# Optimization experiments

Hardware: AMD Instinct MI355X
Metric: run time of the kernel (lower is better)

Reference implementation:

```python
import jax, jax.numpy as jnp
import numpy as np

D_EMBED = 1024
D_CROSS = 768
N_HEADS = 16
D_HEAD = D_EMBED // N_HEADS


def setup_inputs() -> dict:
    key = jax.random.key(0)
    ks = jax.random.split(key, 10)
    s = 0.02
    return {
        "x": jax.random.normal(ks[0], (4, 4096, D_EMBED), dtype=jnp.float32),
        "y": jax.random.normal(ks[1], (4, 1024, D_CROSS), dtype=jnp.float32),
        "Wq": jax.random.normal(ks[2], (D_EMBED, D_EMBED), dtype=jnp.float32) * s,
        "bq": jnp.zeros((D_EMBED,), dtype=jnp.float32),
        "Wk": jax.random.normal(ks[3], (D_CROSS, D_EMBED), dtype=jnp.float32) * s,
        "bk": jnp.zeros((D_EMBED,), dtype=jnp.float32),
        "Wv": jax.random.normal(ks[4], (D_CROSS, D_EMBED), dtype=jnp.float32) * s,
        "bv": jnp.zeros((D_EMBED,), dtype=jnp.float32),
        "Wo": jax.random.normal(ks[5], (D_EMBED, D_EMBED), dtype=jnp.float32) * s,
        "bo": jnp.zeros((D_EMBED,), dtype=jnp.float32),
    }


def reference(x, y, Wq, bq, Wk, bk, Wv, bv, Wo, bo):
    b, sq, _ = x.shape
    skv = y.shape[1]
    # projections
    q = x @ Wq + bq   # [b, sq, d_embed]
    k = y @ Wk + bk   # [b, skv, d_embed]
    v = y @ Wv + bv   # [b, skv, d_embed]
    # split heads: [b, h, s, d_head]
    q = q.reshape(b, sq, N_HEADS, D_HEAD).transpose(0, 2, 1, 3)
    k = k.reshape(b, skv, N_HEADS, D_HEAD).transpose(0, 2, 1, 3)
    v = v.reshape(b, skv, N_HEADS, D_HEAD).transpose(0, 2, 1, 3)
    scale = 1.0 / jnp.sqrt(jnp.float32(D_HEAD))
    scores = jnp.einsum("bhqd,bhkd->bhqk", q, k) * scale
    attn = jax.nn.softmax(scores, axis=-1)
    out = jnp.einsum("bhqk,bhkd->bhqd", attn, v)
    out = out.transpose(0, 2, 1, 3).reshape(b, sq, D_EMBED)
    return out @ Wo + bo
```

## Files before the change

kernel.cpp:

```cpp
#include <hip/hip_runtime.h>

typedef unsigned short ushort_t;
typedef __attribute__((ext_vector_type(8))) __bf16 bf16x8;
typedef __attribute__((ext_vector_type(4))) float floatx4;
typedef __attribute__((ext_vector_type(8))) unsigned short ushortx8;
typedef __attribute__((ext_vector_type(4))) unsigned short ushortx4;
typedef __attribute__((ext_vector_type(4))) short short4v;
typedef __attribute__((ext_vector_type(2))) unsigned uint2v;

__device__ __forceinline__ ushort_t f2bf(float f) {
    union { float f; unsigned u; } v; v.f = f;
    unsigned r = v.u + 0x7fffu + ((v.u >> 16) & 1u);
    return (ushort_t)(r >> 16);
}

__device__ __forceinline__ void gld_lds16(const ushort_t* g, ushort_t* l) {
    __builtin_amdgcn_global_load_lds(
        (const __attribute__((address_space(1))) unsigned*)g,
        (__attribute__((address_space(3))) unsigned*)l, 16, 0, 0);
}

__device__ __forceinline__ unsigned pk_bf16(float a, float b) {
    unsigned ua = __builtin_bit_cast(unsigned, a) + 0x8000u;
    unsigned ub = __builtin_bit_cast(unsigned, b) + 0x8000u;
    return __builtin_amdgcn_perm(ub, ua, 0x07060302u);
}

__global__ __launch_bounds__(256) void prep(
    const float* __restrict__ x, const float* __restrict__ y,
    const float* __restrict__ Wq, const float* __restrict__ Wo,
    const float* __restrict__ Wk, const float* __restrict__ Wv,
    ushort_t* __restrict__ xb, ushort_t* __restrict__ yb,
    ushort_t* __restrict__ Wqt, ushort_t* __restrict__ Wot,
    ushort_t* __restrict__ Wkvt) {
    const int bid = blockIdx.x;
    if (bid < 19456) {
        const int NX = 4194304;
        int i = bid * 256 + threadIdx.x;
        float4 v; ushortx4* dst;
        if (i < NX) { v = ((const float4*)x)[i]; dst = (ushortx4*)xb + i; }
        else        { int j = i - NX; v = ((const float4*)y)[j]; dst = (ushortx4*)yb + j; }
        ushortx4 o;
        o.x = f2bf(v.x); o.y = f2bf(v.y); o.z = f2bf(v.z); o.w = f2bf(v.w);
        *dst = o;
        return;
    }
    __shared__ ushort_t t[32][33];
    const float* W; ushort_t* Wt; int K, n0, k0;
    if (bid < 21504) {
        int tt = bid - 19456;
        W = (tt >> 10) ? Wo : Wq;
        Wt = (tt >> 10) ? Wot : Wqt;
        K = 1024;
        int r = tt & 1023;
        n0 = (r & 31) * 32; k0 = (r >> 5) * 32;
    } else {
        int tt = bid - 21504;
        int z = tt / 768, r = tt - z * 768;
        W = z ? Wv : Wk;
        Wt = Wkvt + (size_t)z * 786432;
        K = 768;
        n0 = (r & 31) * 32; k0 = (r >> 5) * 32;
    }
    const int tx = threadIdx.x & 31, ty = threadIdx.x >> 5;
#pragma unroll
    for (int i = 0; i < 4; ++i)
        t[ty + 8 * i][tx] = f2bf(W[(size_t)(k0 + ty + 8 * i) * 1024 + n0 + tx]);
    __syncthreads();
#pragma unroll
    for (int i = 0; i < 4; ++i)
        Wt[(size_t)(n0 + ty + 8 * i) * K + k0 + tx] = t[tx][ty + 8 * i];
}

__device__ __forceinline__ void gemm_core(
    const ushort_t* __restrict__ A, const ushort_t* __restrict__ Bt,
    int K, int m0, int n0, ushort_t* As, ushort_t* Bs,
    floatx4 (&acc)[4][4], int tid, int wr, int wc, int quad, int l16) {
    const ushort_t* ga0 = A + (size_t)(m0 + (tid >> 2)) * K + (tid & 3) * 8;
    const ushort_t* ga1 = A + (size_t)(m0 + 64 + (tid >> 2)) * K + (tid & 3) * 8;
    const ushort_t* gb0 = Bt + (size_t)(n0 + (tid >> 2)) * K + (tid & 3) * 8;
    const ushort_t* gb1 = Bt + (size_t)(n0 + 64 + (tid >> 2)) * K + (tid & 3) * 8;
    ushort_t* la0 = As + tid * 8;
    ushort_t* la1 = As + (tid + 256) * 8;
    ushort_t* lb0 = Bs + tid * 8;
    ushort_t* lb1 = Bs + (tid + 256) * 8;

    for (int kt = 0; kt < K; kt += 32) {
        __syncthreads();
        gld_lds16(ga0, la0); gld_lds16(ga1, la1);
        gld_lds16(gb0, lb0); gld_lds16(gb1, lb1);
        ga0 += 32; ga1 += 32; gb0 += 32; gb1 += 32;
        __syncthreads();
        bf16x8 af[4], bfr[4];
#pragma unroll
        for (int i = 0; i < 4; ++i)
            af[i] = *(const bf16x8*)(As + (wr * 64 + i * 16 + l16) * 32 + quad * 8);
#pragma unroll
        for (int j = 0; j < 4; ++j)
            bfr[j] = *(const bf16x8*)(Bs + (wc * 64 + j * 16 + l16) * 32 + quad * 8);
#pragma unroll
        for (int i = 0; i < 4; ++i)
#pragma unroll
            for (int j = 0; j < 4; ++j)
                acc[i][j] = __builtin_amdgcn_mfma_f32_16x16x32_bf16(af[i], bfr[j], acc[i][j], 0, 0, 0);
    }
}

__global__ __launch_bounds__(256) void proj(
    const ushort_t* __restrict__ xb, const ushort_t* __restrict__ yb,
    const ushort_t* __restrict__ Wqt, const ushort_t* __restrict__ Wkvt,
    const float* __restrict__ bq, const float* __restrict__ bk, const float* __restrict__ bv,
    ushort_t* __restrict__ Qc, ushort_t* __restrict__ Kc, ushort_t* __restrict__ Vc,
    float qscale) {
    __shared__ __align__(16) ushort_t As[128 * 32];
    __shared__ __align__(16) ushort_t Bs[128 * 32];
    const int tid = threadIdx.x;
    const int lane = tid & 63, w = tid >> 6;
    const int quad = lane >> 4, l16 = lane & 15;
    const int wr = w >> 1, wc = w & 1;
    const int id = blockIdx.x;
    floatx4 acc[4][4] = {};

    if (id < 1024) {
        const int m0 = (id >> 3) * 128, n0 = (id & 7) * 128;
        gemm_core(xb, Wqt, 1024, m0, n0, As, Bs, acc, tid, wr, wc, quad, l16);
#pragma unroll
        for (int i = 0; i < 4; ++i) {
            const int rowb = m0 + wr * 64 + i * 16 + quad * 4;
#pragma unroll
            for (int j = 0; j < 4; ++j) {
                const int col = n0 + wc * 64 + j * 16 + l16;
                const float bval = bq[col];
                const int h = col >> 6, d = col & 63;
                const int b_ = rowb >> 12, q = rowb & 4095;
                ushort_t* base = Qc +
                    (((size_t)b_ * 16 + h) * 32 + (q >> 7)) * 8192 +
                    (d >> 3) * 1024 + (size_t)(q & 127) * 8 + (d & 7);
#pragma unroll
                for (int r = 0; r < 4; ++r)
                    base[r * 8] = f2bf((acc[i][j][r] + bval) * qscale);
            }
        }
    } else {
        const int id2 = id - 1024;
        const int m0 = (id2 & 31) * 128, n0 = (id2 >> 5) * 128;
        gemm_core(yb, Wkvt, 768, m0, n0, As, Bs, acc, tid, wr, wc, quad, l16);
        if (n0 < 1024) {
#pragma unroll
            for (int i = 0; i < 4; ++i) {
                const int rowb = m0 + wr * 64 + i * 16 + quad * 4;
                const int b = rowb >> 10, kvt = (rowb & 1023) >> 6, kvr = rowb & 63;
#pragma unroll
                for (int j = 0; j < 4; ++j) {
                    const int col = n0 + wc * 64 + j * 16 + l16;
                    const int h = col >> 6, d = col & 63;
                    const float bval = bk[col];
                    ushort_t* base = Kc + (((size_t)b * 16 + h) * 16 + kvt) * 4096 +
                                     (d >> 3) * 512 + kvr * 8 + (d & 7);
#pragma unroll
                    for (int r = 0; r < 4; ++r)
                        base[r * 8] = f2bf(acc[i][j][r] + bval);
                }
            }
        } else {
#pragma unroll
            for (int i = 0; i < 4; ++i) {
                const int rowb = m0 + wr * 64 + i * 16 + quad * 4;
                const int b = rowb >> 10, kvt = (rowb & 1023) >> 6, sub = (rowb >> 3) & 7;
#pragma unroll
                for (int j = 0; j < 4; ++j) {
                    const int col = n0 + wc * 64 + j * 16 + l16;
                    const int nc = col - 1024;
                    const int h = nc >> 6, d = nc & 63;
                    const float bval = bv[nc];
                    ushortx4 o;
#pragma unroll
                    for (int r = 0; r < 4; ++r) o[r] = f2bf(acc[i][j][r] + bval);
                    *(ushortx4*)(Vc + (((size_t)b * 16 + h) * 16 + kvt) * 4096 +
                                 sub * 512 + d * 8 + (quad & 1) * 4) = o;
                }
            }
        }
    }
}

__global__ __launch_bounds__(256) void gemm_o(
    const ushort_t* __restrict__ A, const ushort_t* __restrict__ Bt,
    const float* __restrict__ bias, float* __restrict__ C, int N, int K) {
    __shared__ __align__(16) ushort_t As[128 * 32];
    __shared__ __align__(16) ushort_t Bs[128 * 32];
    const int tid = threadIdx.x;
    const int lane = tid & 63, w = tid >> 6;
    const int quad = lane >> 4, l16 = lane & 15;
    const int wr = w >> 1, wc = w & 1;
    const int m0 = blockIdx.x * 128, n0 = blockIdx.y * 128;
    floatx4 acc[4][4] = {};
    gemm_core(A, Bt, K, m0, n0, As, Bs, acc, tid, wr, wc, quad, l16);
#pragma unroll
    for (int i = 0; i < 4; ++i) {
        const int rowb = m0 + wr * 64 + i * 16 + quad * 4;
#pragma unroll
        for (int j = 0; j < 4; ++j) {
            const int col = n0 + wc * 64 + j * 16 + l16;
            const float bval = bias[col];
#pragma unroll
            for (int r = 0; r < 4; ++r)
                C[(size_t)(rowb + r) * N + col] = acc[i][j][r] + bval;
        }
    }
}

__device__ __forceinline__ void stage_kv(const ushort_t* kg, const ushort_t* vg,
                                         ushort_t* dst, int tid) {
#pragma unroll
    for (int i = 0; i < 2; ++i) {
        int s = i * 256 + tid;
        gld_lds16(kg + s * 8, dst + s * 8);
        gld_lds16(vg + s * 8, dst + 4096 + s * 8);
    }
}

__global__ __launch_bounds__(256, 4) void attn_kernel(
    const ushort_t* __restrict__ Qc,
    const ushort_t* __restrict__ Kc,
    const ushort_t* __restrict__ Vc,
    ushort_t* __restrict__ O)
{
    __shared__ __align__(16) ushort_t smem[16384];
    const int tid = threadIdx.x;
    const int w = tid >> 6, lane = tid & 63;
    const int quad = lane >> 4, l16 = lane & 15;
    const int q0 = blockIdx.x * 128;
    const int bh = blockIdx.y, b = bh >> 4;

    const ushort_t* qg = Qc + ((size_t)bh * 32 + blockIdx.x) * 8192;
    bf16x8 qf[2][2];
#pragma unroll
    for (int ks = 0; ks < 2; ++ks)
#pragma unroll
        for (int qt = 0; qt < 2; ++qt)
            qf[ks][qt] = *(const bf16x8*)(qg +
                ((ks * 4 + quad) * 128 + w * 32 + qt * 16 + l16) * 8);

    const ushort_t* kvbase = Kc + (size_t)bh * 65536;
    const ushort_t* vvbase = Vc + (size_t)bh * 65536;
    stage_kv(kvbase, vvbase, smem, tid);
    __syncthreads();

    floatx4 oacc[4][2] = {};
    float lsum[2] = {0.f, 0.f};

    for (int kvt = 0; kvt < 16; ++kvt) {
        const int sel = kvt & 1;
        if (kvt < 15)
            stage_kv(kvbase + (kvt + 1) * 4096, vvbase + (kvt + 1) * 4096,
                     smem + (sel ^ 1) * 8192, tid);
        const ushort_t* pK = smem + sel * 8192;
        const ushort_t* pV = pK + 4096;

        floatx4 st[4][2] = {};
#pragma unroll
        for (int ks = 0; ks < 2; ++ks) {
            bf16x8 ak[4];
#pragma unroll
            for (int m4 = 0; m4 < 4; ++m4)
                ak[m4] = *(const bf16x8*)(pK + ((ks * 4 + quad) * 64 + m4 * 16 + l16) * 8);
#pragma unroll
            for (int m4 = 0; m4 < 4; ++m4)
#pragma unroll
                for (int qt = 0; qt < 2; ++qt)
                    st[m4][qt] = __builtin_amdgcn_mfma_f32_16x16x32_bf16(ak[m4], qf[ks][qt], st[m4][qt], 0, 0, 0);
        }

        uint2v pk[4][2];
#pragma unroll
        for (int qt = 0; qt < 2; ++qt) {
            float acc = 0.f;
#pragma unroll
            for (int m4 = 0; m4 < 4; ++m4) {
                float p0 = __builtin_amdgcn_exp2f(st[m4][qt][0]);
                float p1 = __builtin_amdgcn_exp2f(st[m4][qt][1]);
                float p2 = __builtin_amdgcn_exp2f(st[m4][qt][2]);
                float p3 = __builtin_amdgcn_exp2f(st[m4][qt][3]);
                acc += (p0 + p1) + (p2 + p3);
                pk[m4][qt].x = pk_bf16(p0, p1);
                pk[m4][qt].y = pk_bf16(p2, p3);
            }
            lsum[qt] += acc;
        }

#pragma unroll
        for (int m4 = 0; m4 < 4; ++m4) {
#pragma unroll
            for (int dt = 0; dt < 4; ++dt) {
                short4v av = *(const short4v*)(pV +
                    ((m4 * 2 + (quad >> 1)) * 64 + dt * 16 + l16) * 8 + (quad & 1) * 4);
#pragma unroll
                for (int qt = 0; qt < 2; ++qt) {
                    short4v bp = __builtin_bit_cast(short4v, pk[m4][qt]);
                    oacc[dt][qt] = __builtin_amdgcn_mfma_f32_16x16x16bf16_1k(av, bp, oacc[dt][qt], 0, 0, 0);
                }
            }
        }
        __syncthreads();
    }

    const int h = bh & 15;
    float inv[2];
#pragma unroll
    for (int qt = 0; qt < 2; ++qt) {
        float l = lsum[qt];
        l += __shfl_xor(l, 16, 64);
        l += __shfl_xor(l, 32, 64);
        inv[qt] = 1.0f / l;
    }
#pragma unroll
    for (int dt = 0; dt < 4; ++dt)
#pragma unroll
        for (int qt = 0; qt < 2; ++qt) {
            uint2v o2;
            o2.x = pk_bf16(oacc[dt][qt][0] * inv[qt], oacc[dt][qt][1] * inv[qt]);
            o2.y = pk_bf16(oacc[dt][qt][2] * inv[qt], oacc[dt][qt][3] * inv[qt]);
            *(uint2v*)(smem + (w * 32 + qt * 16 + l16) * 68 + dt * 16 + quad * 4) = o2;
        }
    __syncthreads();
#pragma unroll
    for (int i = 0; i < 8; ++i) {
        int s = i * 256 + tid;
        int row = s >> 4, dc = s & 15;
        ushortx4 v = *(const ushortx4*)(smem + row * 68 + dc * 4);
        *(ushortx4*)(O + (size_t)(b * 4096 + q0 + row) * 1024 + h * 64 + dc * 4) = v;
    }
}

extern "C" void kernel_launch(void* const* d_in, const int* in_sizes, int n_in,
                              void* d_out, int out_size, void* d_ws, size_t ws_size,
                              hipStream_t stream) {
    const float* x  = (const float*)d_in[0];
    const float* y  = (const float*)d_in[1];
    const float* Wq = (const float*)d_in[2];
    const float* bq = (const float*)d_in[3];
    const float* Wk = (const float*)d_in[4];
    const float* bk = (const float*)d_in[5];
    const float* Wv = (const float*)d_in[6];
    const float* bv = (const float*)d_in[7];
    const float* Wo = (const float*)d_in[8];
    const float* bo = (const float*)d_in[9];

    char* ws = (char*)d_ws;
    ushort_t* xb   = (ushort_t*)(ws);
    ushort_t* yb   = (ushort_t*)(ws + 33554432);
    ushort_t* Wqt  = (ushort_t*)(ws + 39845888);
    ushort_t* Wkvt = (ushort_t*)(ws + 41943040);
    ushort_t* Wot  = (ushort_t*)(ws + 45088768);
    ushort_t* Qc   = (ushort_t*)(ws + 47185920);
    ushort_t* Kc   = (ushort_t*)(ws + 80740352);
    ushort_t* Vc   = (ushort_t*)(ws + 89128960);
    ushort_t* Ab   = (ushort_t*)(ws + 97517568);

    const float QSCALE = 0.125f * 1.44269504f;

    prep<<<23040, 256, 0, stream>>>(x, y, Wq, Wo, Wk, Wv, xb, yb, Wqt, Wot, Wkvt);
    proj<<<1536, 256, 0, stream>>>(xb, yb, Wqt, Wkvt, bq, bk, bv, Qc, Kc, Vc, QSCALE);
    attn_kernel<<<dim3(32, 64), 256, 0, stream>>>(Qc, Kc, Vc, Ab);
    gemm_o<<<dim3(128, 8), 256, 0, stream>>>(Ab, Wot, bo, (float*)d_out, 1024, 1024);
}
```

Measured before the change: 365.7 us.

## Use 256x256 triple-buffered GEMM for Q and output projections

Splits the combined projection kernel so the Q projection and the output projection run on a new 256x256-tile, 512-thread GEMM core. The core triple-buffers LDS with direct global-to-LDS loads, uses an XOR swizzle on K chunks, and interleaves the next tile's loads with the MFMA phases, with setprio and a block-index swizzle for L2 locality. The aim is more reuse per loaded byte and less barrier stall in the two large GEMMs. In exchange it launches one more kernel, and with only 256 blocks of 512 threads the load can balance poorly across CUs.

Result: faster. 343.6 us (-6.0%).

```diff
diff --git a/kernel.cpp b/kernel.cpp
--- a/kernel.cpp
+++ b/kernel.cpp
@@ -106,106 +106,193 @@
     }
 }
 
-__global__ __launch_bounds__(256) void proj(
-    const ushort_t* __restrict__ xb, const ushort_t* __restrict__ yb,
-    const ushort_t* __restrict__ Wqt, const ushort_t* __restrict__ Wkvt,
-    const float* __restrict__ bq, const float* __restrict__ bk, const float* __restrict__ bv,
-    ushort_t* __restrict__ Qc, ushort_t* __restrict__ Kc, ushort_t* __restrict__ Vc,
-    float qscale) {
+__global__ __launch_bounds__(256) void proj_kv(
+    const ushort_t* __restrict__ yb, const ushort_t* __restrict__ Wkvt,
+    const float* __restrict__ bk, const float* __restrict__ bv,
+    ushort_t* __restrict__ Kc, ushort_t* __restrict__ Vc) {
     __shared__ __align__(16) ushort_t As[128 * 32];
     __shared__ __align__(16) ushort_t Bs[128 * 32];
     const int tid = threadIdx.x;
     const int lane = tid & 63, w = tid >> 6;
     const int quad = lane >> 4, l16 = lane & 15;
     const int wr = w >> 1, wc = w & 1;
-    const int id = blockIdx.x;
+    const int id2 = blockIdx.x;
+    const int m0 = (id2 & 31) * 128, n0 = (id2 >> 5) * 128;
     floatx4 acc[4][4] = {};
-
-    if (id < 1024) {
-        const int m0 = (id >> 3) * 128, n0 = (id & 7) * 128;
-        gemm_core(xb, Wqt, 1024, m0, n0, As, Bs, acc, tid, wr, wc, quad, l16);
+    gemm_core(yb, Wkvt, 768, m0, n0, As, Bs, acc, tid, wr, wc, quad, l16);
+    if (n0 < 1024) {
 #pragma unroll
         for (int i = 0; i < 4; ++i) {
             const int rowb = m0 + wr * 64 + i * 16 + quad * 4;
+            const int b = rowb >> 10, kvt = (rowb & 1023) >> 6, kvr = rowb & 63;
 #pragma unroll
             for (int j = 0; j < 4; ++j) {
                 const int col = n0 + wc * 64 + j * 16 + l16;
-                const float bval = bq[col];
                 const int h = col >> 6, d = col & 63;
-                const int b_ = rowb >> 12, q = rowb & 4095;
-                ushort_t* base = Qc +
-                    (((size_t)b_ * 16 + h) * 32 + (q >> 7)) * 8192 +
-                    (d >> 3) * 1024 + (size_t)(q & 127) * 8 + (d & 7);
+                const float bval = bk[col];
+                ushort_t* base = Kc + (((size_t)b * 16 + h) * 16 + kvt) * 4096 +
+                                 (d >> 3) * 512 + kvr * 8 + (d & 7);
 #pragma unroll
                 for (int r = 0; r < 4; ++r)
-                    base[r * 8] = f2bf((acc[i][j][r] + bval) * qscale);
+                    base[r * 8] = f2bf(acc[i][j][r] + bval);
             }
         }
     } else {
-        const int id2 = id - 1024;
-        const int m0 = (id2 & 31) * 128, n0 = (id2 >> 5) * 128;
-        gemm_core(yb, Wkvt, 768, m0, n0, As, Bs, acc, tid, wr, wc, quad, l16);
-        if (n0 < 1024) {
-#pragma unroll
-            for (int i = 0; i < 4; ++i) {
-                const int rowb = m0 + wr * 64 + i * 16 + quad * 4;
-                const int b = rowb >> 10, kvt = (rowb & 1023) >> 6, kvr = rowb & 63;
-#pragma unroll
-                for (int j = 0; j < 4; ++j) {
-                    const int col = n0 + wc * 64 + j * 16 + l16;
-                    const int h = col >> 6, d = col & 63;
-                    const float bval = bk[col];
-                    ushort_t* base = Kc + (((size_t)b * 16 + h) * 16 + kvt) * 4096 +
-                                     (d >> 3) * 512 + kvr * 8 + (d & 7);
-#pragma unroll
-                    for (int r = 0; r < 4; ++r)
-                        base[r * 8] = f2bf(acc[i][j][r] + bval);
-                }
+#pragma unroll
+        for (int i = 0; i < 4; ++i) {
+            const int rowb = m0 + wr * 64 + i * 16 + quad * 4;
+            const int b = rowb >> 10, kvt = (rowb & 1023) >> 6, sub = (rowb >> 3) & 7;
+#pragma unroll
+            for (int j = 0; j < 4; ++j) {
+                const int col = n0 + wc * 64 + j * 16 + l16;
+                const int nc = col - 1024;
+                const int h = nc >> 6, d = nc & 63;
+                const float bval = bv[nc];
+                ushortx4 o;
+#pragma unroll
+                for (int r = 0; r < 4; ++r) o[r] = f2bf(acc[i][j][r] + bval);
+                *(ushortx4*)(Vc + (((size_t)b * 16 + h) * 16 + kvt) * 4096 +
+                             sub * 512 + d * 8 + (quad & 1) * 4) = o;
             }
-        } else {
-#pragma unroll
-            for (int i = 0; i < 4; ++i) {
-                const int rowb = m0 + wr * 64 + i * 16 + quad * 4;
-                const int b = rowb >> 10, kvt = (rowb & 1023) >> 6, sub = (rowb >> 3) & 7;
-#pragma unroll
-                for (int j = 0; j < 4; ++j) {
-                    const int col = n0 + wc * 64 + j * 16 + l16;
-                    const int nc = col - 1024;
-                    const int h = nc >> 6, d = nc & 63;
-                    const float bval = bv[nc];
-                    ushortx4 o;
-#pragma unroll
-                    for (int r = 0; r < 4; ++r) o[r] = f2bf(acc[i][j][r] + bval);
-                    *(ushortx4*)(Vc + (((size_t)b * 16 + h) * 16 + kvt) * 4096 +
-                                 sub * 512 + d * 8 + (quad & 1) * 4) = o;
-                }
-            }
-        }
-    }
-}
-
-__global__ __launch_bounds__(256) void gemm_o(
+        }
+    }
+}
+
+__device__ __forceinline__ void gemm256_core(
     const ushort_t* __restrict__ A, const ushort_t* __restrict__ Bt,
-    const float* __restrict__ bias, float* __restrict__ C, int N, int K) {
-    __shared__ __align__(16) ushort_t As[128 * 32];
-    __shared__ __align__(16) ushort_t Bs[128 * 32];
+    ushort_t* lds, floatx4 (&acc)[8][4],
+    int m0, int n0, int tid, int wr, int wc, int quad, int l16) {
+    const int K = 1024, NT = 32;
+    const int cx = (quad ^ (l16 & 3)) * 8;
+
+    const int ra = tid >> 2;
+    const int ka = (tid & 3) ^ (ra & 3);
+    const ushort_t* gA0 = A + (size_t)(m0 + ra) * K + ka * 8;
+    const ushort_t* gA1 = gA0 + (size_t)128 * K;
+    const ushort_t* gB0 = Bt + (size_t)(n0 + ra) * K + ka * 8;
+    const ushort_t* gB1 = gB0 + (size_t)128 * K;
+    const int dA0 = tid * 8, dA1 = tid * 8 + 4096;
+    const int dB0 = 8192 + tid * 8, dB1 = 8192 + tid * 8 + 4096;
+
+#pragma unroll
+    for (int pt = 0; pt < 2; ++pt) {
+        ushort_t* d = lds + pt * 16384;
+        gld_lds16(gA0, d + dA0); gld_lds16(gA1, d + dA1);
+        gld_lds16(gB0, d + dB0); gld_lds16(gB1, d + dB1);
+        gA0 += 32; gA1 += 32; gB0 += 32; gB1 += 32;
+    }
+
+    int cur = 0, nxt = 2;
+    for (int t = 0; t < NT; ++t) {
+        if (t < NT - 1) asm volatile("s_waitcnt vmcnt(4)" ::: "memory");
+        else            asm volatile("s_waitcnt vmcnt(0)" ::: "memory");
+        __builtin_amdgcn_s_barrier();
+        __builtin_amdgcn_sched_barrier(0);
+        const ushort_t* Abase = lds + cur * 16384;
+        const ushort_t* Bbase = Abase + 8192;
+        ushort_t* dn = lds + nxt * 16384;
+
+        bf16x8 af[4], bfr[4];
+#pragma unroll
+        for (int fr = 0; fr < 4; ++fr)
+            af[fr] = *(const bf16x8*)(Abase + (wr * 128 + fr * 16 + l16) * 32 + cx);
+#pragma unroll
+        for (int fc = 0; fc < 4; ++fc)
+            bfr[fc] = *(const bf16x8*)(Bbase + (wc * 64 + fc * 16 + l16) * 32 + cx);
+        if (t + 2 < NT) { gld_lds16(gA0, dn + dA0); gld_lds16(gA1, dn + dA1); }
+        asm volatile("s_waitcnt lgkmcnt(0)" ::: "memory");
+        __builtin_amdgcn_sched_barrier(0);
+        __builtin_amdgcn_s_setprio(1);
+#pragma unroll
+        for (int fr = 0; fr < 4; ++fr)
+#pragma unroll
+            for (int fc = 0; fc < 4; ++fc)
+                acc[fr][fc] = __builtin_amdgcn_mfma_f32_16x16x32_bf16(af[fr], bfr[fc], acc[fr][fc], 0, 0, 0);
+        __builtin_amdgcn_s_setprio(0);
+        __builtin_amdgcn_sched_barrier(0);
+        __builtin_amdgcn_s_barrier();
+        __builtin_amdgcn_sched_barrier(0);
+
+#pragma unroll
+        for (int fr = 0; fr < 4; ++fr)
+            af[fr] = *(const bf16x8*)(Abase + (wr * 128 + 64 + fr * 16 + l16) * 32 + cx);
+        if (t + 2 < NT) {
+            gld_lds16(gB0, dn + dB0); gld_lds16(gB1, dn + dB1);
+            gA0 += 32; gA1 += 32; gB0 += 32; gB1 += 32;
+        }
+        asm volatile("s_waitcnt lgkmcnt(0)" ::: "memory");
+        __builtin_amdgcn_sched_barrier(0);
+        __builtin_amdgcn_s_setprio(1);
+#pragma unroll
+        for (int fr = 0; fr < 4; ++fr)
+#pragma unroll
+            for (int fc = 0; fc < 4; ++fc)
+                acc[fr + 4][fc] = __builtin_amdgcn_mfma_f32_16x16x32_bf16(af[fr], bfr[fc], acc[fr + 4][fc], 0, 0, 0);
+        __builtin_amdgcn_s_setprio(0);
+        cur = cur == 2 ? 0 : cur + 1;
+        nxt = nxt == 2 ? 0 : nxt + 1;
+    }
+}
+
+__global__ __launch_bounds__(512, 2) void gemm256_q(
+    const ushort_t* __restrict__ A, const ushort_t* __restrict__ Bt,
+    const float* __restrict__ bq, ushort_t* __restrict__ Qc, float qscale) {
+    __shared__ __align__(16) ushort_t lds[49152];
     const int tid = threadIdx.x;
     const int lane = tid & 63, w = tid >> 6;
     const int quad = lane >> 4, l16 = lane & 15;
-    const int wr = w >> 1, wc = w & 1;
-    const int m0 = blockIdx.x * 128, n0 = blockIdx.y * 128;
-    floatx4 acc[4][4] = {};
-    gemm_core(A, Bt, K, m0, n0, As, Bs, acc, tid, wr, wc, quad, l16);
-#pragma unroll
-    for (int i = 0; i < 4; ++i) {
-        const int rowb = m0 + wr * 64 + i * 16 + quad * 4;
-#pragma unroll
-        for (int j = 0; j < 4; ++j) {
-            const int col = n0 + wc * 64 + j * 16 + l16;
+    const int wr = w >> 2, wc = w & 3;
+    const int bid = blockIdx.x;
+    const int swz = (bid & 7) * 32 + (bid >> 3);
+    const int m0 = (swz >> 2) * 256, n0 = (swz & 3) * 256;
+
+    floatx4 acc[8][4] = {};
+    gemm256_core(A, Bt, lds, acc, m0, n0, tid, wr, wc, quad, l16);
+
+#pragma unroll
+    for (int fr = 0; fr < 8; ++fr) {
+        const int rowb = m0 + wr * 128 + fr * 16 + quad * 4;
+        const int b_ = rowb >> 12, q = rowb & 4095;
+#pragma unroll
+        for (int fc = 0; fc < 4; ++fc) {
+            const int col = n0 + wc * 64 + fc * 16 + l16;
+            const float bval = bq[col];
+            const int h = col >> 6, d = col & 63;
+            ushort_t* base = Qc +
+                (((size_t)b_ * 16 + h) * 32 + (q >> 7)) * 8192 +
+                (d >> 3) * 1024 + (size_t)(q & 127) * 8 + (d & 7);
+#pragma unroll
+            for (int r = 0; r < 4; ++r)
+                base[r * 8] = f2bf((acc[fr][fc][r] + bval) * qscale);
+        }
+    }
+}
+
+__global__ __launch_bounds__(512, 2) void gemm256_o(
+    const ushort_t* __restrict__ A, const ushort_t* __restrict__ Bt,
+    const float* __restrict__ bias, float* __restrict__ C) {
+    __shared__ __align__(16) ushort_t lds[49152];
+    const int tid = threadIdx.x;
+    const int lane = tid & 63, w = tid >> 6;
+    const int quad = lane >> 4, l16 = lane & 15;
+    const int wr = w >> 2, wc = w & 3;
+    const int bid = blockIdx.x;
+    const int swz = (bid & 7) * 32 + (bid >> 3);
+    const int m0 = (swz >> 2) * 256, n0 = (swz & 3) * 256;
+
+    floatx4 acc[8][4] = {};
+    gemm256_core(A, Bt, lds, acc, m0, n0, tid, wr, wc, quad, l16);
+
+#pragma unroll
+    for (int fr = 0; fr < 8; ++fr) {
+        const int rowb = m0 + wr * 128 + fr * 16 + quad * 4;
+#pragma unroll
+        for (int fc = 0; fc < 4; ++fc) {
+            const int col = n0 + wc * 64 + fc * 16 + l16;
             const float bval = bias[col];
 #pragma unroll
             for (int r = 0; r < 4; ++r)
-                C[(size_t)(rowb + r) * N + col] = acc[i][j][r] + bval;
+                C[(size_t)(rowb + r) * 1024 + col] = acc[fr][fc][r] + bval;
         }
     }
 }
@@ -361,7 +448,8 @@
     const float QSCALE = 0.125f * 1.44269504f;
 
     prep<<<23040, 256, 0, stream>>>(x, y, Wq, Wo, Wk, Wv, xb, yb, Wqt, Wot, Wkvt);
-    proj<<<1536, 256, 0, stream>>>(xb, yb, Wqt, Wkvt, bq, bk, bv, Qc, Kc, Vc, QSCALE);
+    gemm256_q<<<256, 512, 0, stream>>>(xb, Wqt, bq, Qc, QSCALE);
+    proj_kv<<<512, 256, 0, stream>>>(yb, Wkvt, bk, bv, Kc, Vc);
     attn_kernel<<<dim3(32, 64), 256, 0, stream>>>(Qc, Kc, Vc, Ab);
-    gemm_o<<<dim3(128, 8), 256, 0, stream>>>(Ab, Wot, bo, (float*)d_out, 1024, 1024);
-}
+    gemm256_o<<<256, 512, 0, stream>>>(Ab, Wot, bo, (float*)d_out);
+}
```

## Use 256x128 triple-buffered GEMM tiles with LDS swizzle for projections and output

Applied to the files above, without the earlier changes.

Replaces the 128x128 double-sync GEMM core with a 512-thread 256x128 tile core. It uses a three-stage global-to-LDS pipeline with explicit vmcnt/lgkmcnt waits, an XOR-swizzled LDS layout to avoid bank conflicts, split MFMA phases with raised priority, and block-index swizzling for L2 locality. The goal is to hide global load latency and cut LDS and sync overhead in the Q/K/V projection and output GEMMs. The attention launch is also split into two half-grid launches, which adds a launch. The larger LDS footprint may reduce occupancy.

Measured after the change: 335.7 us. 8.2% less time.

```diff
diff --git a/kernel.cpp b/kernel.cpp
--- a/kernel.cpp
+++ b/kernel.cpp
@@ -72,67 +72,101 @@
         Wt[(size_t)(n0 + ty + 8 * i) * K + k0 + tx] = t[tx][ty + 8 * i];
 }
 
-__device__ __forceinline__ void gemm_core(
+__device__ __forceinline__ void gemm_tile_core(
     const ushort_t* __restrict__ A, const ushort_t* __restrict__ Bt,
-    int K, int m0, int n0, ushort_t* As, ushort_t* Bs,
-    floatx4 (&acc)[4][4], int tid, int wr, int wc, int quad, int l16) {
-    const ushort_t* ga0 = A + (size_t)(m0 + (tid >> 2)) * K + (tid & 3) * 8;
-    const ushort_t* ga1 = A + (size_t)(m0 + 64 + (tid >> 2)) * K + (tid & 3) * 8;
-    const ushort_t* gb0 = Bt + (size_t)(n0 + (tid >> 2)) * K + (tid & 3) * 8;
-    const ushort_t* gb1 = Bt + (size_t)(n0 + 64 + (tid >> 2)) * K + (tid & 3) * 8;
-    ushort_t* la0 = As + tid * 8;
-    ushort_t* la1 = As + (tid + 256) * 8;
-    ushort_t* lb0 = Bs + tid * 8;
-    ushort_t* lb1 = Bs + (tid + 256) * 8;
-
-    for (int kt = 0; kt < K; kt += 32) {
-        __syncthreads();
-        gld_lds16(ga0, la0); gld_lds16(ga1, la1);
-        gld_lds16(gb0, lb0); gld_lds16(gb1, lb1);
-        ga0 += 32; ga1 += 32; gb0 += 32; gb1 += 32;
-        __syncthreads();
-        bf16x8 af[4], bfr[4];
-#pragma unroll
-        for (int i = 0; i < 4; ++i)
-            af[i] = *(const bf16x8*)(As + (wr * 64 + i * 16 + l16) * 32 + quad * 8);
-#pragma unroll
-        for (int j = 0; j < 4; ++j)
-            bfr[j] = *(const bf16x8*)(Bs + (wc * 64 + j * 16 + l16) * 32 + quad * 8);
-#pragma unroll
-        for (int i = 0; i < 4; ++i)
-#pragma unroll
-            for (int j = 0; j < 4; ++j)
-                acc[i][j] = __builtin_amdgcn_mfma_f32_16x16x32_bf16(af[i], bfr[j], acc[i][j], 0, 0, 0);
-    }
-}
-
-__global__ __launch_bounds__(256) void proj(
+    int K, int NT, ushort_t* lds, floatx4 (&acc)[4][4],
+    int m0, int n0, int tid, int wr, int wc, int quad, int l16) {
+    const int cx = (quad ^ ((l16 >> 1) & 3)) * 8;
+
+    const int ra = tid >> 2;
+    const int ka = (tid & 3) ^ ((tid >> 3) & 3);
+    const ushort_t* gA0 = A + (size_t)(m0 + ra) * K + ka * 8;
+    const ushort_t* gA1 = gA0 + (size_t)128 * K;
+    const ushort_t* gB0 = Bt + (size_t)(n0 + ra) * K + ka * 8;
+    const int dA0 = tid * 8, dA1 = tid * 8 + 4096, dB0 = 8192 + tid * 8;
+
+#pragma unroll
+    for (int pt = 0; pt < 2; ++pt) {
+        ushort_t* d = lds + pt * 12288;
+        gld_lds16(gA0, d + dA0); gld_lds16(gA1, d + dA1); gld_lds16(gB0, d + dB0);
+        gA0 += 32; gA1 += 32; gB0 += 32;
+    }
+
+    int cur = 0, nxt = 2;
+    for (int t = 0; t < NT; ++t) {
+        if (t < NT - 1) asm volatile("s_waitcnt vmcnt(3)" ::: "memory");
+        else            asm volatile("s_waitcnt vmcnt(0)" ::: "memory");
+        __builtin_amdgcn_s_barrier();
+        __builtin_amdgcn_sched_barrier(0);
+        const ushort_t* Abase = lds + cur * 12288;
+        const ushort_t* Bbase = Abase + 8192;
+        ushort_t* dn = lds + nxt * 12288;
+
+        bf16x8 af0, af1, af2, af3, bfr[4];
+        af0 = *(const bf16x8*)(Abase + (wr * 64 + l16) * 32 + cx);
+        af1 = *(const bf16x8*)(Abase + (wr * 64 + 16 + l16) * 32 + cx);
+#pragma unroll
+        for (int fc = 0; fc < 4; ++fc)
+            bfr[fc] = *(const bf16x8*)(Bbase + (wc * 64 + fc * 16 + l16) * 32 + cx);
+        __builtin_amdgcn_sched_barrier(0);
+        if (t + 2 < NT) {
+            gld_lds16(gA0, dn + dA0); gld_lds16(gA1, dn + dA1); gld_lds16(gB0, dn + dB0);
+            gA0 += 32; gA1 += 32; gB0 += 32;
+        }
+        __builtin_amdgcn_sched_barrier(0);
+        af2 = *(const bf16x8*)(Abase + (wr * 64 + 32 + l16) * 32 + cx);
+        af3 = *(const bf16x8*)(Abase + (wr * 64 + 48 + l16) * 32 + cx);
+        asm volatile("s_waitcnt lgkmcnt(2)" ::: "memory");
+        __builtin_amdgcn_sched_barrier(0);
+        __builtin_amdgcn_s_setprio(1);
+#pragma unroll
+        for (int fc = 0; fc < 4; ++fc) {
+            acc[0][fc] = __builtin_amdgcn_mfma_f32_16x16x32_bf16(af0, bfr[fc], acc[0][fc], 0, 0, 0);
+            acc[1][fc] = __builtin_amdgcn_mfma_f32_16x16x32_bf16(af1, bfr[fc], acc[1][fc], 0, 0, 0);
+        }
+        __builtin_amdgcn_s_setprio(0);
+        asm volatile("s_waitcnt lgkmcnt(0)" ::: "memory");
+        __builtin_amdgcn_sched_barrier(0);
+        __builtin_amdgcn_s_setprio(1);
+#pragma unroll
+        for (int fc = 0; fc < 4; ++fc) {
+            acc[2][fc] = __builtin_amdgcn_mfma_f32_16x16x32_bf16(af2, bfr[fc], acc[2][fc], 0, 0, 0);
+            acc[3][fc] = __builtin_amdgcn_mfma_f32_16x16x32_bf16(af3, bfr[fc], acc[3][fc], 0, 0, 0);
+        }
+        __builtin_amdgcn_s_setprio(0);
+        __builtin_amdgcn_sched_barrier(0);
+        cur = cur == 2 ? 0 : cur + 1;
+        nxt = nxt == 2 ? 0 : nxt + 1;
+    }
+}
+
+__global__ __launch_bounds__(512, 4) void proj256(
     const ushort_t* __restrict__ xb, const ushort_t* __restrict__ yb,
     const ushort_t* __restrict__ Wqt, const ushort_t* __restrict__ Wkvt,
     const float* __restrict__ bq, const float* __restrict__ bk, const float* __restrict__ bv,
     ushort_t* __restrict__ Qc, ushort_t* __restrict__ Kc, ushort_t* __restrict__ Vc,
     float qscale) {
-    __shared__ __align__(16) ushort_t As[128 * 32];
-    __shared__ __align__(16) ushort_t Bs[128 * 32];
+    __shared__ __align__(16) ushort_t lds[36864];
     const int tid = threadIdx.x;
     const int lane = tid & 63, w = tid >> 6;
     const int quad = lane >> 4, l16 = lane & 15;
     const int wr = w >> 1, wc = w & 1;
-    const int id = blockIdx.x;
+    const int bid = blockIdx.x;
     floatx4 acc[4][4] = {};
 
-    if (id < 1024) {
-        const int m0 = (id >> 3) * 128, n0 = (id & 7) * 128;
-        gemm_core(xb, Wqt, 1024, m0, n0, As, Bs, acc, tid, wr, wc, quad, l16);
+    if (bid < 512) {
+        const int swz = (bid & 7) * 64 + (bid >> 3);
+        const int m0 = (swz >> 3) * 256, n0 = (swz & 7) * 128;
+        gemm_tile_core(xb, Wqt, 1024, 32, lds, acc, m0, n0, tid, wr, wc, quad, l16);
 #pragma unroll
         for (int i = 0; i < 4; ++i) {
             const int rowb = m0 + wr * 64 + i * 16 + quad * 4;
+            const int b_ = rowb >> 12, q = rowb & 4095;
 #pragma unroll
             for (int j = 0; j < 4; ++j) {
                 const int col = n0 + wc * 64 + j * 16 + l16;
                 const float bval = bq[col];
                 const int h = col >> 6, d = col & 63;
-                const int b_ = rowb >> 12, q = rowb & 4095;
                 ushort_t* base = Qc +
                     (((size_t)b_ * 16 + h) * 32 + (q >> 7)) * 8192 +
                     (d >> 3) * 1024 + (size_t)(q & 127) * 8 + (d & 7);
@@ -142,9 +176,10 @@
             }
         }
     } else {
-        const int id2 = id - 1024;
-        const int m0 = (id2 & 31) * 128, n0 = (id2 >> 5) * 128;
-        gemm_core(yb, Wkvt, 768, m0, n0, As, Bs, acc, tid, wr, wc, quad, l16);
+        const int id2 = bid - 512;
+        const int swz = (id2 & 7) * 32 + (id2 >> 3);
+        const int m0 = (swz >> 4) * 256, n0 = (swz & 15) * 128;
+        gemm_tile_core(yb, Wkvt, 768, 24, lds, acc, m0, n0, tid, wr, wc, quad, l16);
         if (n0 < 1024) {
 #pragma unroll
             for (int i = 0; i < 4; ++i) {
@@ -184,18 +219,21 @@
     }
 }
 
-__global__ __launch_bounds__(256) void gemm_o(
+__global__ __launch_bounds__(512, 4) void gemm256_o(
     const ushort_t* __restrict__ A, const ushort_t* __restrict__ Bt,
-    const float* __restrict__ bias, float* __restrict__ C, int N, int K) {
-    __shared__ __align__(16) ushort_t As[128 * 32];
-    __shared__ __align__(16) ushort_t Bs[128 * 32];
+    const float* __restrict__ bias, float* __restrict__ C) {
+    __shared__ __align__(16) ushort_t lds[36864];
     const int tid = threadIdx.x;
     const int lane = tid & 63, w = tid >> 6;
     const int quad = lane >> 4, l16 = lane & 15;
     const int wr = w >> 1, wc = w & 1;
-    const int m0 = blockIdx.x * 128, n0 = blockIdx.y * 128;
+    const int bid = blockIdx.x;
+    const int swz = (bid & 7) * 64 + (bid >> 3);
+    const int m0 = (swz >> 3) * 256, n0 = (swz & 7) * 128;
+
     floatx4 acc[4][4] = {};
-    gemm_core(A, Bt, K, m0, n0, As, Bs, acc, tid, wr, wc, quad, l16);
+    gemm_tile_core(A, Bt, 1024, 32, lds, acc, m0, n0, tid, wr, wc, quad, l16);
+
 #pragma unroll
     for (int i = 0; i < 4; ++i) {
         const int rowb = m0 + wr * 64 + i * 16 + quad * 4;
@@ -205,7 +243,7 @@
             const float bval = bias[col];
 #pragma unroll
             for (int r = 0; r < 4; ++r)
-                C[(size_t)(rowb + r) * N + col] = acc[i][j][r] + bval;
+                C[(size_t)(rowb + r) * 1024 + col] = acc[i][j][r] + bval;
         }
     }
 }
@@ -224,14 +262,15 @@
     const ushort_t* __restrict__ Qc,
     const ushort_t* __restrict__ Kc,
     const ushort_t* __restrict__ Vc,
-    ushort_t* __restrict__ O)
+    ushort_t* __restrict__ O,
+    const int bh0)
 {
     __shared__ __align__(16) ushort_t smem[16384];
     const int tid = threadIdx.x;
     const int w = tid >> 6, lane = tid & 63;
     const int quad = lane >> 4, l16 = lane & 15;
     const int q0 = blockIdx.x * 128;
-    const int bh = blockIdx.y, b = bh >> 4;
+    const int bh = blockIdx.y + bh0, b = bh >> 4;
 
     const ushort_t* qg = Qc + ((size_t)bh * 32 + blockIdx.x) * 8192;
     bf16x8 qf[2][2];
@@ -361,7 +400,8 @@
     const float QSCALE = 0.125f * 1.44269504f;
 
     prep<<<23040, 256, 0, stream>>>(x, y, Wq, Wo, Wk, Wv, xb, yb, Wqt, Wot, Wkvt);
-    proj<<<1536, 256, 0, stream>>>(xb, yb, Wqt, Wkvt, bq, bk, bv, Qc, Kc, Vc, QSCALE);
-    attn_kernel<<<dim3(32, 64), 256, 0, stream>>>(Qc, Kc, Vc, Ab);
-    gemm_o<<<dim3(128, 8), 256, 0, stream>>>(Ab, Wot, bo, (float*)d_out, 1024, 1024);
-}
+    proj256<<<768, 512, 0, stream>>>(xb, yb, Wqt, Wkvt, bq, bk, bv, Qc, Kc, Vc, QSCALE);
+    attn_kernel<<<dim3(32, 32), 256, 0, stream>>>(Qc, Kc, Vc, Ab, 0);
+    attn_kernel<<<dim3(32, 32), 256, 0, stream>>>(Qc, Kc, Vc, Ab, 32);
+    gemm256_o<<<512, 512, 0, stream>>>(Ab, Wot, bo, (float*)d_out);
+}
```
